# Performance work log

Measured on AMD Instinct MI355X. Metric: run time of the kernel, lower is better.

Reference implementation:

```python
import jax, jax.numpy as jnp
import numpy as np

BSZ, L, H, P = 8, 4096, 512, 256  # batch, seq len, features, complex state dim (conj_sym)
DT_MIN, DT_MAX = 1e-3, 1e-1


def setup_inputs() -> dict:
    key = jax.random.key(0)
    k_u, k_B, k_C, k_D, k_dt = jax.random.split(key, 5)
    u = jax.random.normal(k_u, (BSZ, L, H), dtype=jnp.float32)
    # HiPPO-like stable init for the diagonal state matrix
    Lambda_re = -0.5 * jnp.ones((P,), dtype=jnp.float32)
    Lambda_im = jnp.pi * jnp.arange(P, dtype=jnp.float32)
    # lecun-normal-ish scaling for real/imag parts of B (fan_in = H) and C (fan_in = P)
    B = jax.random.normal(k_B, (P, H, 2), dtype=jnp.float32) / jnp.sqrt(2.0 * H)
    C = jax.random.normal(k_C, (H, P, 2), dtype=jnp.float32) / jnp.sqrt(2.0 * P)
    D = jax.random.normal(k_D, (H,), dtype=jnp.float32)
    log_step = jax.random.uniform(k_dt, (P, 1), dtype=jnp.float32,
                                  minval=jnp.log(DT_MIN), maxval=jnp.log(DT_MAX))
    return {"u": u, "Lambda_re": Lambda_re, "Lambda_im": Lambda_im,
            "B": B, "C": C, "D": D, "log_step": log_step}


def _binop(q_i, q_j):
    """Associative binary operator for diagonal linear recurrence."""
    A_i, b_i = q_i
    A_j, b_j = q_j
    return (A_j * A_i, A_j * b_i + b_j)


def reference(u, Lambda_re, Lambda_im, B, C, D, log_step):
    # --- setup / discretization (zero-order hold) ---
    Lambda = (Lambda_re + 1j * Lambda_im).astype(jnp.complex64)      # (P,)
    B_tilde = (B[..., 0] + 1j * B[..., 1]).astype(jnp.complex64)     # (P,H)
    C_tilde = (C[..., 0] + 1j * C[..., 1]).astype(jnp.complex64)     # (H,P)
    step = jnp.exp(log_step[:, 0])                                   # (P,)
    Lambda_bar = jnp.exp(Lambda * step)                              # (P,)
    B_bar = ((Lambda_bar - 1.0) / Lambda)[:, None] * B_tilde         # (P,H)

    # --- parallel scan over the sequence (diagonal SSM) ---
    Bu = jnp.einsum('blh,ph->blp', u, B_bar)                         # (B,L,P) complex64
    Lam = jnp.broadcast_to(Lambda_bar, Bu.shape)                     # (B,L,P)
    _, xs = jax.lax.associative_scan(_binop, (Lam, Bu), axis=1)      # (B,L,P)

    # --- emissions (factor 2 from conjugate symmetry) + feedthrough ---
    ys = 2.0 * jnp.einsum('blp,hp->blh', xs, C_tilde).real + D * u   # (B,L,H)
    return jax.nn.gelu(ys)
```

## Files before the change

kernel.cpp:

```cpp
#include <hip/hip_runtime.h>
#include <cstdint>
#include <cstddef>

typedef unsigned short u16;
typedef short short8 __attribute__((ext_vector_type(8)));
typedef float floatx4 __attribute__((ext_vector_type(4)));

#define DEVINL __device__ __forceinline__

static constexpr int BSZ = 8, SEQL = 4096, H = 512, P = 256;
static constexpr int M = BSZ * SEQL;
static constexpr int KD = 512;
static constexpr int ND = 512;
static constexpr int CHUNK = 64;
static constexpr int NCH = SEQL / CHUNK;

DEVINL u16 f2bf(float f) {
  union { float f; unsigned u; } v; v.f = f;
  unsigned r = (v.u + 0x7fffu + ((v.u >> 16) & 1u)) >> 16;
  return (u16)r;
}
DEVINL float bf2f(u16 h) {
  union { unsigned u; float f; } v; v.u = ((unsigned)h) << 16; return v.f;
}

DEVINL void gload_lds16(const void* g, void* l) {
  __builtin_amdgcn_global_load_lds(
      (const __attribute__((address_space(1))) unsigned*)g,
      (__attribute__((address_space(3))) unsigned*)l, 16, 0, 0);
}

__global__ void setup_kernel(const float* __restrict__ Lre, const float* __restrict__ Lim,
                             const float* __restrict__ logstep,
                             float2* __restrict__ lam, float2* __restrict__ ffac) {
  int p = threadIdx.x;
  if (p >= P) return;
  float lr = Lre[p], li = Lim[p];
  float st = expf(logstep[p]);
  float mag = expf(lr * st);
  float ang = li * st;
  float cr = mag * cosf(ang);
  float ci = mag * sinf(ang);
  lam[p] = make_float2(cr, ci);
  float a = cr - 1.0f, b = ci;
  float den = lr * lr + li * li;
  float fr = (a * lr + b * li) / den;
  float fi = (b * lr - a * li) / den;
  ffac[p] = make_float2(fr, fi);
}

__global__ void bt1_kernel(const float2* __restrict__ Bin,
                           const float2* __restrict__ ffac,
                           u16* __restrict__ bt1) {
  int idx = blockIdx.x * 256 + threadIdx.x;
  int p = idx / H, h = idx % H;
  float2 bv = Bin[(size_t)p * H + h];
  float2 f = ffac[p];
  float br = f.x * bv.x - f.y * bv.y;
  float bi = f.x * bv.y + f.y * bv.x;
  bt1[(size_t)(2 * p) * H + h]     = f2bf(br);
  bt1[(size_t)(2 * p + 1) * H + h] = f2bf(bi);
}

__global__ void bt2_kernel(const float* __restrict__ Cin, u16* __restrict__ bt2) {
  int idx = blockIdx.x * 256 + threadIdx.x;
  float c = Cin[idx];
  float v = (idx & 1) ? -2.0f * c : 2.0f * c;
  bt2[idx] = f2bf(v);
}

__global__ __launch_bounds__(256, 3) void gemm0(const float* __restrict__ Af32,
                                                const u16* __restrict__ Bt,
                                                u16* __restrict__ outBf) {
  __shared__ float Asf[2][128 * 32];
  __shared__ u16   Bs[2][128 * 32];
  const int tid = threadIdx.x;
  const int bm = blockIdx.x, bn = blockIdx.y;
  const int wave = tid >> 6, lane = tid & 63;
  const int quad = lane >> 4, l16 = lane & 15;
  const int wm = (wave & 1) << 6, wn = (wave >> 1) << 6;

  floatx4 acc[4][4] = {};

  const float* Ab = Af32 + (size_t)bm * 128 * KD;
  const u16*   Bb = Bt + (size_t)bn * 128 * KD;
  const int srowA = tid >> 3;
  const int scolA = (tid & 7) << 2;
  const int srowB = tid >> 2;
  const int scolB = (tid & 3) << 3;

#define STAGE0(buf, kofs)                                                                     \
  do {                                                                                        \
    gload_lds16(Ab + (size_t)srowA * KD + (kofs) + scolA,        &Asf[buf][tid * 4]);         \
    gload_lds16(Ab + (size_t)(srowA + 32) * KD + (kofs) + scolA, &Asf[buf][1024 + tid * 4]);  \
    gload_lds16(Ab + (size_t)(srowA + 64) * KD + (kofs) + scolA, &Asf[buf][2048 + tid * 4]);  \
    gload_lds16(Ab + (size_t)(srowA + 96) * KD + (kofs) + scolA, &Asf[buf][3072 + tid * 4]);  \
    gload_lds16(Bb + (size_t)srowB * KD + (kofs) + scolB,        &Bs[buf][tid * 8]);          \
    gload_lds16(Bb + (size_t)(srowB + 64) * KD + (kofs) + scolB, &Bs[buf][2048 + tid * 8]);   \
  } while (0)

  STAGE0(0, 0);
  asm volatile("s_waitcnt vmcnt(0)" ::: "memory");
  __builtin_amdgcn_sched_barrier(0);
  __builtin_amdgcn_s_barrier();

  int cur = 0;
  for (int k0 = 0; k0 < KD; k0 += 32) {
    if (k0 + 32 < KD) STAGE0(cur ^ 1, k0 + 32);

    short8 af[4], bfr[4];
#pragma unroll
    for (int t = 0; t < 4; t++) {
      const float* ap = &Asf[cur][(wm + t * 16 + l16) * 32 + quad * 8];
      float4 a0 = *(const float4*)ap;
      float4 a1 = *(const float4*)(ap + 4);
      af[t][0] = (short)f2bf(a0.x); af[t][1] = (short)f2bf(a0.y);
      af[t][2] = (short)f2bf(a0.z); af[t][3] = (short)f2bf(a0.w);
      af[t][4] = (short)f2bf(a1.x); af[t][5] = (short)f2bf(a1.y);
      af[t][6] = (short)f2bf(a1.z); af[t][7] = (short)f2bf(a1.w);
    }
#pragma unroll
    for (int t = 0; t < 4; t++)
      bfr[t] = *(const short8*)&Bs[cur][(wn + t * 16 + l16) * 32 + quad * 8];

    asm volatile("s_waitcnt lgkmcnt(0)" ::: "memory");
    __builtin_amdgcn_sched_barrier(0);

    __builtin_amdgcn_s_setprio(1);
#pragma unroll
    for (int tm = 0; tm < 4; tm++)
#pragma unroll
      for (int tn = 0; tn < 4; tn++)
        acc[tm][tn] = __builtin_amdgcn_mfma_f32_16x16x32_bf16(af[tm], bfr[tn], acc[tm][tn], 0, 0, 0);
    __builtin_amdgcn_s_setprio(0);

    asm volatile("s_waitcnt vmcnt(0)" ::: "memory");
    __builtin_amdgcn_sched_barrier(0);
    __builtin_amdgcn_s_barrier();
    cur ^= 1;
  }
#undef STAGE0

  const int row_base = bm * 128 + wm + quad * 4;
  const int col_base = bn * 128 + wn + l16;
#pragma unroll
  for (int tm = 0; tm < 4; tm++)
#pragma unroll
    for (int tn = 0; tn < 4; tn++) {
      int n = col_base + tn * 16;
#pragma unroll
      for (int r = 0; r < 4; r++) {
        int m = row_base + tm * 16 + r;
        outBf[(size_t)m * ND + n] = f2bf(acc[tm][tn][r]);
      }
    }
}

__global__ __launch_bounds__(256, 4) void gemm1(const u16* __restrict__ A,
                                                const u16* __restrict__ Bt,
                                                float* __restrict__ outF,
                                                const float* __restrict__ Dv,
                                                const float* __restrict__ U32) {
  __shared__ u16 As[2][128 * 32];
  __shared__ u16 Bs[2][128 * 32];
  const int tid = threadIdx.x;
  const int bm = blockIdx.x, bn = blockIdx.y;
  const int wave = tid >> 6, lane = tid & 63;
  const int quad = lane >> 4, l16 = lane & 15;
  const int wm = (wave & 1) << 6, wn = (wave >> 1) << 6;

  floatx4 acc[4][4] = {};

  const u16* Ab = A + (size_t)bm * 128 * KD;
  const u16* Bb = Bt + (size_t)bn * 128 * KD;
  const int srow = tid >> 2;
  const int scol = (tid & 3) << 3;

#define STAGE1(buf, kofs)                                                                  \
  do {                                                                                     \
    gload_lds16(Ab + (size_t)srow * KD + (kofs) + scol,        &As[buf][tid * 8]);         \
    gload_lds16(Ab + (size_t)(srow + 64) * KD + (kofs) + scol, &As[buf][2048 + tid * 8]);  \
    gload_lds16(Bb + (size_t)srow * KD + (kofs) + scol,        &Bs[buf][tid * 8]);         \
    gload_lds16(Bb + (size_t)(srow + 64) * KD + (kofs) + scol, &Bs[buf][2048 + tid * 8]);  \
  } while (0)

  STAGE1(0, 0);
  asm volatile("s_waitcnt vmcnt(0)" ::: "memory");
  __builtin_amdgcn_sched_barrier(0);
  __builtin_amdgcn_s_barrier();

  int cur = 0;
  for (int k0 = 0; k0 < KD; k0 += 32) {
    if (k0 + 32 < KD) STAGE1(cur ^ 1, k0 + 32);

    short8 af[4], bfr[4];
#pragma unroll
    for (int t = 0; t < 4; t++)
      af[t] = *(const short8*)&As[cur][(wm + t * 16 + l16) * 32 + quad * 8];
#pragma unroll
    for (int t = 0; t < 4; t++)
      bfr[t] = *(const short8*)&Bs[cur][(wn + t * 16 + l16) * 32 + quad * 8];

    asm volatile("s_waitcnt lgkmcnt(0)" ::: "memory");
    __builtin_amdgcn_sched_barrier(0);

    __builtin_amdgcn_s_setprio(1);
#pragma unroll
    for (int tm = 0; tm < 4; tm++)
#pragma unroll
      for (int tn = 0; tn < 4; tn++)
        acc[tm][tn] = __builtin_amdgcn_mfma_f32_16x16x32_bf16(af[tm], bfr[tn], acc[tm][tn], 0, 0, 0);
    __builtin_amdgcn_s_setprio(0);

    asm volatile("s_waitcnt vmcnt(0)" ::: "memory");
    __builtin_amdgcn_sched_barrier(0);
    __builtin_amdgcn_s_barrier();
    cur ^= 1;
  }
#undef STAGE1

  const int row_base = bm * 128 + wm + quad * 4;
  const int col_base = bn * 128 + wn + l16;
  float dv[4];
#pragma unroll
  for (int tn = 0; tn < 4; tn++) dv[tn] = Dv[col_base + tn * 16];
#pragma unroll
  for (int tm = 0; tm < 4; tm++)
#pragma unroll
    for (int tn = 0; tn < 4; tn++) {
      int n = col_base + tn * 16;
#pragma unroll
      for (int r = 0; r < 4; r++) {
        int m = row_base + tm * 16 + r;
        float ys = acc[tm][tn][r] + dv[tn] * U32[(size_t)m * ND + n];
        float zz = ys + 0.044715f * (ys * ys * ys);
        float e = __builtin_amdgcn_exp2f(-2.3022082f * zz);
        outF[(size_t)m * ND + n] = ys * __builtin_amdgcn_rcpf(1.0f + e);
      }
    }
}

__global__ __launch_bounds__(256) void scan_carry(const u16* __restrict__ Bu,
                                                  const float2* __restrict__ lam,
                                                  float2* __restrict__ carry) {
  int p = threadIdx.x;
  int c = blockIdx.x;
  int b = blockIdx.y;
  float2 lm = lam[p];
  float xr = 0.f, xi = 0.f;
  const u16* base = Bu + ((size_t)b * SEQL + (size_t)c * CHUNK) * 512 + 2 * p;
  for (int l = 0; l < CHUNK; l++) {
    unsigned w = *(const unsigned*)(base + (size_t)l * 512);
    float br = bf2f((u16)(w & 0xffffu));
    float bi = bf2f((u16)(w >> 16));
    float nr = lm.x * xr - lm.y * xi + br;
    float ni = lm.x * xi + lm.y * xr + bi;
    xr = nr; xi = ni;
  }
  carry[((size_t)b * NCH + c) * P + p] = make_float2(xr, xi);
}

__global__ __launch_bounds__(256) void scan_prefix(const float2* __restrict__ carry,
                                                   const float2* __restrict__ lam,
                                                   float2* __restrict__ prefix) {
  int p = threadIdx.x;
  int b = blockIdx.x;
  float2 lm = lam[p];
  float ar = lm.x, ai = lm.y;
  for (int i = 0; i < 6; i++) { float nr = ar * ar - ai * ai, ni = 2.f * ar * ai; ar = nr; ai = ni; }
  float pr = 0.f, pi = 0.f;
  for (int c = 0; c < NCH; c++) {
    prefix[((size_t)b * NCH + c) * P + p] = make_float2(pr, pi);
    float2 ca = carry[((size_t)b * NCH + c) * P + p];
    float nr = ar * pr - ai * pi + ca.x;
    float ni = ar * pi + ai * pr + ca.y;
    pr = nr; pi = ni;
  }
}

__global__ __launch_bounds__(256) void scan_apply(u16* __restrict__ Bu,
                                                  const float2* __restrict__ lam,
                                                  const float2* __restrict__ prefix) {
  int p = threadIdx.x;
  int c = blockIdx.x;
  int b = blockIdx.y;
  float2 lm = lam[p];
  float2 pf = prefix[((size_t)b * NCH + c) * P + p];
  float xr = pf.x, xi = pf.y;
  u16* base = Bu + ((size_t)b * SEQL + (size_t)c * CHUNK) * 512 + 2 * p;
  for (int l = 0; l < CHUNK; l++) {
    unsigned* addr = (unsigned*)(base + (size_t)l * 512);
    unsigned w = *addr;
    float br = bf2f((u16)(w & 0xffffu));
    float bi = bf2f((u16)(w >> 16));
    float nr = lm.x * xr - lm.y * xi + br;
    float ni = lm.x * xi + lm.y * xr + bi;
    xr = nr; xi = ni;
    *addr = (unsigned)f2bf(nr) | ((unsigned)f2bf(ni) << 16);
  }
}

extern "C" void kernel_launch(void* const* d_in, const int* in_sizes, int n_in,
                              void* d_out, int out_size, void* d_ws, size_t ws_size,
                              hipStream_t stream) {
  const float* u      = (const float*)d_in[0];
  const float* Lre    = (const float*)d_in[1];
  const float* Lim    = (const float*)d_in[2];
  const float* Bin    = (const float*)d_in[3];
  const float* Cin    = (const float*)d_in[4];
  const float* Dv     = (const float*)d_in[5];
  const float* lstep  = (const float*)d_in[6];
  float* out          = (float*)d_out;

  char* ws = (char*)d_ws;
  float2* lam    = (float2*)(ws + 0);
  float2* ffac   = (float2*)(ws + 2048);
  u16*    bt1    = (u16*)   (ws + 4096);
  u16*    bt2    = (u16*)   (ws + 528384);
  u16*    Bu     = (u16*)   (ws + 1052672);
  float2* carry  = (float2*)(ws + 34607104);
  float2* prefix = (float2*)(ws + 35655680);

  setup_kernel<<<1, 256, 0, stream>>>(Lre, Lim, lstep, lam, ffac);
  bt1_kernel<<<(P * H) / 256, 256, 0, stream>>>((const float2*)Bin, ffac, bt1);
  bt2_kernel<<<(H * P * 2) / 256, 256, 0, stream>>>(Cin, bt2);

  gemm0<<<dim3(M / 128, ND / 128), 256, 0, stream>>>(u, bt1, Bu);

  scan_carry <<<dim3(NCH, BSZ), 256, 0, stream>>>(Bu, lam, carry);
  scan_prefix<<<BSZ, 256, 0, stream>>>(carry, lam, prefix);
  scan_apply <<<dim3(NCH, BSZ), 256, 0, stream>>>(Bu, lam, prefix);

  gemm1<<<dim3(M / 128, ND / 128), 256, 0, stream>>>(Bu, bt2, out, Dv, u);
}
```

Before: 211.3 us.

## Fuse prep kernels, fold prefix scan into apply, swizzle gemm0 A tile in LDS

Merges the setup, B-transform and C-transform kernels into one prep launch that recomputes the discretised Lambda per element, and recomputes Lambda inside the scan kernels instead of reading it from workspace. The separate serial scan_prefix kernel is removed: each scan_apply block recomputes its own chunk prefix by walking all earlier carries, which cuts launches and a serial dependency but adds redundant work that grows with chunk index. The gemm0 fp32 A tile in LDS is XOR-swizzled to reduce bank conflicts on the fragment reads.

```diff
diff --git a/kernel.cpp b/kernel.cpp
--- a/kernel.cpp
+++ b/kernel.cpp
@@ -30,43 +30,43 @@
       (__attribute__((address_space(3))) unsigned*)l, 16, 0, 0);
 }
 
-__global__ void setup_kernel(const float* __restrict__ Lre, const float* __restrict__ Lim,
-                             const float* __restrict__ logstep,
-                             float2* __restrict__ lam, float2* __restrict__ ffac) {
-  int p = threadIdx.x;
-  if (p >= P) return;
+DEVINL float2 lam_of(int p, const float* __restrict__ Lre, const float* __restrict__ Lim,
+                     const float* __restrict__ lstep) {
   float lr = Lre[p], li = Lim[p];
-  float st = expf(logstep[p]);
+  float st = expf(lstep[p]);
   float mag = expf(lr * st);
   float ang = li * st;
-  float cr = mag * cosf(ang);
-  float ci = mag * sinf(ang);
-  lam[p] = make_float2(cr, ci);
-  float a = cr - 1.0f, b = ci;
-  float den = lr * lr + li * li;
-  float fr = (a * lr + b * li) / den;
-  float fi = (b * lr - a * li) / den;
-  ffac[p] = make_float2(fr, fi);
-}
-
-__global__ void bt1_kernel(const float2* __restrict__ Bin,
-                           const float2* __restrict__ ffac,
-                           u16* __restrict__ bt1) {
-  int idx = blockIdx.x * 256 + threadIdx.x;
-  int p = idx / H, h = idx % H;
-  float2 bv = Bin[(size_t)p * H + h];
-  float2 f = ffac[p];
-  float br = f.x * bv.x - f.y * bv.y;
-  float bi = f.x * bv.y + f.y * bv.x;
-  bt1[(size_t)(2 * p) * H + h]     = f2bf(br);
-  bt1[(size_t)(2 * p + 1) * H + h] = f2bf(bi);
-}
-
-__global__ void bt2_kernel(const float* __restrict__ Cin, u16* __restrict__ bt2) {
-  int idx = blockIdx.x * 256 + threadIdx.x;
-  float c = Cin[idx];
-  float v = (idx & 1) ? -2.0f * c : 2.0f * c;
-  bt2[idx] = f2bf(v);
+  return make_float2(mag * cosf(ang), mag * sinf(ang));
+}
+
+__global__ void prep_kernel(const float2* __restrict__ Bin, const float* __restrict__ Cin,
+                            const float* __restrict__ Lre, const float* __restrict__ Lim,
+                            const float* __restrict__ lstep,
+                            u16* __restrict__ bt1, u16* __restrict__ bt2) {
+  int bid = blockIdx.x;
+  if (bid < 512) {
+    int idx = bid * 256 + threadIdx.x;
+    int p = idx / H, h = idx % H;
+    float lr = Lre[p], li = Lim[p];
+    float st = expf(lstep[p]);
+    float mag = expf(lr * st);
+    float ang = li * st;
+    float cr = mag * cosf(ang), ci = mag * sinf(ang);
+    float a = cr - 1.0f, b = ci;
+    float den = lr * lr + li * li;
+    float fr = (a * lr + b * li) / den;
+    float fi = (b * lr - a * li) / den;
+    float2 bv = Bin[(size_t)p * H + h];
+    float br = fr * bv.x - fi * bv.y;
+    float bi = fr * bv.y + fi * bv.x;
+    bt1[(size_t)(2 * p) * H + h]     = f2bf(br);
+    bt1[(size_t)(2 * p + 1) * H + h] = f2bf(bi);
+  } else {
+    int idx = (bid - 512) * 256 + threadIdx.x;
+    float c = Cin[idx];
+    float v = (idx & 1) ? -2.0f * c : 2.0f * c;
+    bt2[idx] = f2bf(v);
+  }
 }
 
 __global__ __launch_bounds__(256, 3) void gemm0(const float* __restrict__ Af32,
@@ -85,7 +85,7 @@
   const float* Ab = Af32 + (size_t)bm * 128 * KD;
   const u16*   Bb = Bt + (size_t)bn * 128 * KD;
   const int srowA = tid >> 3;
-  const int scolA = (tid & 7) << 2;
+  const int scolA = (((tid & 7) ^ ((tid >> 3) & 7)) << 2);
   const int srowB = tid >> 2;
   const int scolB = (tid & 3) << 3;
 
@@ -104,6 +104,9 @@
   __builtin_amdgcn_sched_barrier(0);
   __builtin_amdgcn_s_barrier();
 
+  const int c0 = ((quad << 1) ^ (l16 & 7));
+  const int c1 = c0 ^ 1;
+
   int cur = 0;
   for (int k0 = 0; k0 < KD; k0 += 32) {
     if (k0 + 32 < KD) STAGE0(cur ^ 1, k0 + 32);
@@ -111,9 +114,9 @@
     short8 af[4], bfr[4];
 #pragma unroll
     for (int t = 0; t < 4; t++) {
-      const float* ap = &Asf[cur][(wm + t * 16 + l16) * 32 + quad * 8];
-      float4 a0 = *(const float4*)ap;
-      float4 a1 = *(const float4*)(ap + 4);
+      const float* rowp = &Asf[cur][(wm + t * 16 + l16) * 32];
+      float4 a0 = *(const float4*)(rowp + c0 * 4);
+      float4 a1 = *(const float4*)(rowp + c1 * 4);
       af[t][0] = (short)f2bf(a0.x); af[t][1] = (short)f2bf(a0.y);
       af[t][2] = (short)f2bf(a0.z); af[t][3] = (short)f2bf(a0.w);
       af[t][4] = (short)f2bf(a1.x); af[t][5] = (short)f2bf(a1.y);
@@ -241,12 +244,14 @@
 }
 
 __global__ __launch_bounds__(256) void scan_carry(const u16* __restrict__ Bu,
-                                                  const float2* __restrict__ lam,
+                                                  const float* __restrict__ Lre,
+                                                  const float* __restrict__ Lim,
+                                                  const float* __restrict__ lstep,
                                                   float2* __restrict__ carry) {
   int p = threadIdx.x;
   int c = blockIdx.x;
   int b = blockIdx.y;
-  float2 lm = lam[p];
+  float2 lm = lam_of(p, Lre, Lim, lstep);
   float xr = 0.f, xi = 0.f;
   const u16* base = Bu + ((size_t)b * SEQL + (size_t)c * CHUNK) * 512 + 2 * p;
   for (int l = 0; l < CHUNK; l++) {
@@ -260,33 +265,40 @@
   carry[((size_t)b * NCH + c) * P + p] = make_float2(xr, xi);
 }
 
-__global__ __launch_bounds__(256) void scan_prefix(const float2* __restrict__ carry,
-                                                   const float2* __restrict__ lam,
-                                                   float2* __restrict__ prefix) {
+__global__ __launch_bounds__(256) void scan_apply(u16* __restrict__ Bu,
+                                                  const float* __restrict__ Lre,
+                                                  const float* __restrict__ Lim,
+                                                  const float* __restrict__ lstep,
+                                                  const float2* __restrict__ carry) {
   int p = threadIdx.x;
-  int b = blockIdx.x;
-  float2 lm = lam[p];
+  int c = blockIdx.x;
+  int b = blockIdx.y;
+  float2 lm = lam_of(p, Lre, Lim, lstep);
   float ar = lm.x, ai = lm.y;
   for (int i = 0; i < 6; i++) { float nr = ar * ar - ai * ai, ni = 2.f * ar * ai; ar = nr; ai = ni; }
   float pr = 0.f, pi = 0.f;
-  for (int c = 0; c < NCH; c++) {
-    prefix[((size_t)b * NCH + c) * P + p] = make_float2(pr, pi);
-    float2 ca = carry[((size_t)b * NCH + c) * P + p];
-    float nr = ar * pr - ai * pi + ca.x;
-    float ni = ar * pi + ai * pr + ca.y;
-    pr = nr; pi = ni;
-  }
-}
-
-__global__ __launch_bounds__(256) void scan_apply(u16* __restrict__ Bu,
-                                                  const float2* __restrict__ lam,
-                                                  const float2* __restrict__ prefix) {
-  int p = threadIdx.x;
-  int c = blockIdx.x;
-  int b = blockIdx.y;
-  float2 lm = lam[p];
-  float2 pf = prefix[((size_t)b * NCH + c) * P + p];
-  float xr = pf.x, xi = pf.y;
+  const float2* cb_base = carry + (size_t)b * NCH * P + p;
+  for (int j0 = 0; j0 < c; j0 += 16) {
+    float2 cb[16];
+#pragma unroll
+    for (int t = 0; t < 16; t++) {
+      int j = j0 + t;
+      int jc = j < c ? j : c - 1;
+      cb[t] = cb_base[(size_t)jc * P];
+    }
+#pragma unroll
+    for (int t = 0; t < 16; t++) {
+      bool real = (j0 + t) < c;
+      float mr = real ? ar : 1.0f;
+      float mi = real ? ai : 0.0f;
+      float cx = real ? cb[t].x : 0.0f;
+      float cy = real ? cb[t].y : 0.0f;
+      float nr = mr * pr - mi * pi + cx;
+      float ni = mr * pi + mi * pr + cy;
+      pr = nr; pi = ni;
+    }
+  }
+  float xr = pr, xi = pi;
   u16* base = Bu + ((size_t)b * SEQL + (size_t)c * CHUNK) * 512 + 2 * p;
   for (int l = 0; l < CHUNK; l++) {
     unsigned* addr = (unsigned*)(base + (size_t)l * 512);
@@ -313,23 +325,17 @@
   float* out          = (float*)d_out;
 
   char* ws = (char*)d_ws;
-  float2* lam    = (float2*)(ws + 0);
-  float2* ffac   = (float2*)(ws + 2048);
-  u16*    bt1    = (u16*)   (ws + 4096);
-  u16*    bt2    = (u16*)   (ws + 528384);
-  u16*    Bu     = (u16*)   (ws + 1052672);
-  float2* carry  = (float2*)(ws + 34607104);
-  float2* prefix = (float2*)(ws + 35655680);
-
-  setup_kernel<<<1, 256, 0, stream>>>(Lre, Lim, lstep, lam, ffac);
-  bt1_kernel<<<(P * H) / 256, 256, 0, stream>>>((const float2*)Bin, ffac, bt1);
-  bt2_kernel<<<(H * P * 2) / 256, 256, 0, stream>>>(Cin, bt2);
+  u16*    bt1    = (u16*)   (ws + 0);
+  u16*    bt2    = (u16*)   (ws + 524288);
+  u16*    Bu     = (u16*)   (ws + 1048576);
+  float2* carry  = (float2*)(ws + 34603008);
+
+  prep_kernel<<<1536, 256, 0, stream>>>((const float2*)Bin, Cin, Lre, Lim, lstep, bt1, bt2);
 
   gemm0<<<dim3(M / 128, ND / 128), 256, 0, stream>>>(u, bt1, Bu);
 
-  scan_carry <<<dim3(NCH, BSZ), 256, 0, stream>>>(Bu, lam, carry);
-  scan_prefix<<<BSZ, 256, 0, stream>>>(carry, lam, prefix);
-  scan_apply <<<dim3(NCH, BSZ), 256, 0, stream>>>(Bu, lam, prefix);
+  scan_carry<<<dim3(NCH, BSZ), 256, 0, stream>>>(Bu, Lre, Lim, lstep, carry);
+  scan_apply<<<dim3(NCH, BSZ), 256, 0, stream>>>(Bu, Lre, Lim, lstep, carry);
 
   gemm1<<<dim3(M / 128, ND / 128), 256, 0, stream>>>(Bu, bt2, out, Dv, u);
 }
```

New measurement: 208.5 us. About the same (-1.3%).
